# Optimization experiments

Measured on AMD Instinct MI355X. Metric: run time of the kernel, lower is better.

## Reference

```python
import jax, jax.numpy as jnp
import numpy as np

TOP_K = 2  # moe_top_k


def setup_inputs() -> dict:
    key = jax.random.key(0)
    k0, k1, k2, k3 = jax.random.split(key, 4)
    SL, BS, H, F, E = 2048, 4, 1024, 1024, 8
    x = jax.random.normal(k0, (SL, BS, H), dtype=jnp.float32)
    w_router = jax.random.normal(k1, (H, E), dtype=jnp.float32) * 0.02
    w1 = jax.random.normal(k2, (E, H, F), dtype=jnp.float32) * 0.02  # per-expert map weights
    w2 = jax.random.normal(k3, (E, F, H), dtype=jnp.float32) * 0.02  # per-expert reduce weights
    return {"x": x, "w_router": w_router, "w1": w1, "w2": w2}


def reference(x, w_router, w1, w2):
    # dMoA forward: router -> dropless dispatch -> per-expert map GEMM ->
    # per-expert reduce GEMM -> expert-weighted combine. Dropless = no capacity
    # dropping, so a dense all-experts compute + per-token selection is exactly
    # equivalent in math to the sort/gather/grouped-GEMM/scatter pipeline.
    sl, bs, h = x.shape
    E = w1.shape[0]
    xt = x.reshape(-1, h)  # [T, H], T = sl*bs
    T = xt.shape[0]

    # LearnedRouter: softmax over expert logits, then top-k weights/indices
    scores = jax.nn.softmax(xt @ w_router, axis=-1)       # [T, E]
    expert_weights, top_experts = jax.lax.top_k(scores, TOP_K)  # [T, K]

    # load-balancing loss (router.loss): E * sum_e f_e * p_e
    onehot = jax.nn.one_hot(top_experts, E, dtype=xt.dtype)  # [T, K, E]
    tokens_frac = onehot.sum(axis=(0, 1)) / (T * TOP_K)      # f_e
    probs_mean = scores.mean(axis=0)                         # p_e
    loss = E * jnp.sum(tokens_frac * probs_mean)

    # map: per-expert linear H->F, select the top-k experts' outputs per token
    y_all = jnp.einsum('th,ehf->tef', xt, w1)                 # [T, E, F]
    h_tk = jnp.take_along_axis(y_all, top_experts[:, :, None], axis=1)  # [T, K, F]

    # reduce: weighted scatter-combine, then per-expert linear F->H
    hw = jnp.einsum('tke,tk,tkf->tef', onehot, expert_weights, h_tk)  # [T, E, F]
    out = jnp.einsum('tef,efh->th', hw, w2)                   # [T, H]
    return out.reshape(sl, bs, h), loss
```

## Files before the change

### kernel.cpp

```cpp
#include <hip/hip_runtime.h>
#include <hip/hip_bf16.h>
#include <stdint.h>


#define HD 1024
#define FD 1024
#define EN 8

typedef __attribute__((ext_vector_type(8))) short bf16x8;
typedef __attribute__((ext_vector_type(4))) float f32x4;

__device__ __forceinline__ void gload16(const void* g, void* l) {
    __builtin_amdgcn_global_load_lds(
        (const __attribute__((address_space(1))) unsigned int*)g,
        (__attribute__((address_space(3))) unsigned int*)l, 16, 0, 0);
}

__device__ __forceinline__ bf16x8 ds_read128(const short* p) {
    bf16x8 r;
    asm volatile("ds_read_b128 %0, %1"
                 : "=v"(r)
                 : "v"((const __attribute__((address_space(3))) short*)p));
    return r;
}

__device__ __forceinline__ ushort f2bf(float v) {
    __hip_bfloat16 h = __float2bfloat16(v);
    return *(ushort*)&h;
}
__device__ __forceinline__ float bf2f(ushort u) {
    unsigned int w = ((unsigned int)u) << 16;
    float f; __builtin_memcpy(&f, &w, 4); return f;
}

__global__ __launch_bounds__(256) void router_kernel(
    const float* __restrict__ x, const float* __restrict__ wrt,
    ushort* __restrict__ xb,
    int* __restrict__ top_e, float* __restrict__ top_w,
    int* __restrict__ counts, float* __restrict__ probsum)
{
    __shared__ int   cnt_s[EN];
    __shared__ float ps_s[EN];
    int tid = threadIdx.x;
    if (tid < EN) { cnt_s[tid] = 0; ps_s[tid] = 0.f; }
    __syncthreads();

    int wid = tid >> 6, lane = tid & 63;
    int t = blockIdx.x * 4 + wid;
    const float4* xr4 = (const float4*)(x + (size_t)t * HD);
    ushort4* xbo = (ushort4*)(xb + (size_t)t * HD);
    float acc[EN];
#pragma unroll
    for (int e = 0; e < EN; e++) acc[e] = 0.f;
#pragma unroll
    for (int it = 0; it < 4; it++) {
        float4 xv = xr4[it * 64 + lane];
        ushort4 o; o.x = f2bf(xv.x); o.y = f2bf(xv.y); o.z = f2bf(xv.z); o.w = f2bf(xv.w);
        xbo[it * 64 + lane] = o;
        int h0 = it * 256 + lane * 4;
        float xs[4] = {xv.x, xv.y, xv.z, xv.w};
#pragma unroll
        for (int j = 0; j < 4; j++) {
            const float4* wp = (const float4*)(wrt + (size_t)(h0 + j) * EN);
            float4 wa = wp[0], wb = wp[1];
            acc[0] += xs[j] * wa.x; acc[1] += xs[j] * wa.y;
            acc[2] += xs[j] * wa.z; acc[3] += xs[j] * wa.w;
            acc[4] += xs[j] * wb.x; acc[5] += xs[j] * wb.y;
            acc[6] += xs[j] * wb.z; acc[7] += xs[j] * wb.w;
        }
    }
#pragma unroll
    for (int off = 32; off >= 1; off >>= 1) {
#pragma unroll
        for (int e = 0; e < EN; e++) acc[e] += __shfl_xor(acc[e], off, 64);
    }
    if (lane == 0) {
        float m = acc[0];
#pragma unroll
        for (int e = 1; e < EN; e++) m = fmaxf(m, acc[e]);
        float p[EN], s = 0.f;
#pragma unroll
        for (int e = 0; e < EN; e++) { p[e] = expf(acc[e] - m); s += p[e]; }
        float inv = 1.f / s;
#pragma unroll
        for (int e = 0; e < EN; e++) p[e] *= inv;
        int e0 = 0;
#pragma unroll
        for (int e = 1; e < EN; e++) if (p[e] > p[e0]) e0 = e;
        int e1 = (e0 == 0) ? 1 : 0;
#pragma unroll
        for (int e = 0; e < EN; e++) {
            if (e == e0) continue;
            if (p[e] > p[e1]) e1 = e;
        }
        top_e[t * 2] = e0;  top_e[t * 2 + 1] = e1;
        top_w[t * 2] = p[e0]; top_w[t * 2 + 1] = p[e1];
        atomicAdd(&cnt_s[e0], 1); atomicAdd(&cnt_s[e1], 1);
#pragma unroll
        for (int e = 0; e < EN; e++) atomicAdd(&ps_s[e], p[e]);
    }
    __syncthreads();
    if (tid < EN) {
        atomicAdd(&counts[tid], cnt_s[tid]);
        atomicAdd(&probsum[tid], ps_s[tid]);
    }
}

__global__ void prep_kernel(const int* __restrict__ counts,
                            const float* __restrict__ probsum,
                            int* __restrict__ offs, float* __restrict__ loss_out)
{
    int off = 0; float loss = 0.f;
    for (int e = 0; e < EN; e++) {
        offs[e] = off;
        off += counts[e];
        loss += ((float)counts[e] / 16384.f) * (probsum[e] / 8192.f);
    }
    offs[EN] = off;
    *loss_out = 8.f * loss;
}

__global__ __launch_bounds__(256) void dispatch_kernel(
    const int* __restrict__ top_e, const float* __restrict__ top_w,
    const int* __restrict__ offs, int* __restrict__ cursor,
    int* __restrict__ tok_list, float* __restrict__ w_list)
{
    int t = blockIdx.x * 256 + threadIdx.x;
    int lane = threadIdx.x & 63;
#pragma unroll
    for (int k = 0; k < 2; k++) {
        int e = top_e[t * 2 + k];
        int idx = 0;
#pragma unroll
        for (int ex = 0; ex < EN; ex++) {
            unsigned long long m = __ballot(e == ex);
            if (e == ex) {
                int cnt = __popcll(m);
                int leader = __ffsll(m) - 1;
                int pos = 0;
                if (lane == leader) pos = atomicAdd(&cursor[ex * 16], cnt);
                pos = __shfl(pos, leader, 64);
                int rank = __popcll(m & ((1ull << lane) - 1ull));
                idx = offs[ex] + pos + rank;
            }
        }
        tok_list[idx] = t * 2 + k;
        w_list[idx] = top_w[t * 2 + k];
    }
}

__global__ __launch_bounds__(256) void transpose_conv_kernel(
    const float* __restrict__ w1, const float* __restrict__ w2,
    ushort* __restrict__ w1b, ushort* __restrict__ w2b)
{
    __shared__ float tile[32][33];
    int bid = blockIdx.x;
    const float* in; ushort* outp;
    if (bid >= 8192) { in = w2; outp = w2b; bid -= 8192; }
    else             { in = w1; outp = w1b; }
    int e  = bid >> 10;
    int t2 = bid & 1023;
    int tb = t2 >> 5;
    int ta = t2 & 31;
    const float* pin = in + ((size_t)e << 20);
    ushort* pout = outp + ((size_t)e << 20);
    int tx = threadIdx.x & 31, ty = threadIdx.x >> 5;
#pragma unroll
    for (int j = 0; j < 4; j++)
        tile[ty + j * 8][tx] = pin[(size_t)(ta * 32 + ty + j * 8) * 1024 + tb * 32 + tx];
    __syncthreads();
#pragma unroll
    for (int j = 0; j < 4; j++)
        pout[(size_t)(tb * 32 + ty + j * 8) * 1024 + ta * 32 + tx] =
            f2bf(tile[tx][ty + j * 8]);
}


#define RDA(ml_, ks_) ds_read128(&lA[cur][wm * 128 + (ml_) * 16 + lo][(((ks_) * 4 + hi) ^ rx) << 3])
#define RDB(n_, ks_)  ds_read128(&lB[cur][wn * 64  + (n_) * 16 + lo][(((ks_) * 4 + hi) ^ rx) << 3])
#define MFMA_Q(mb_, nb_)                                                      \
    do {                                                                      \
        _Pragma("unroll") for (int ks = 0; ks < 2; ks++)                      \
        _Pragma("unroll") for (int ml = 0; ml < 4; ml++)                      \
        _Pragma("unroll") for (int nl = 0; nl < 2; nl++)                      \
            acc[(mb_) + ml][(nb_) + nl] =                                     \
                __builtin_amdgcn_mfma_f32_16x16x32_bf16(                      \
                    a[ml][ks], b[(nb_) + nl][ks], acc[(mb_) + ml][(nb_) + nl],\
                    0, 0, 0);                                                 \
    } while (0)
#define LGK0_FENCE()                                                          \
    do { asm volatile("s_waitcnt lgkmcnt(0)");                                \
         __builtin_amdgcn_sched_barrier(0); } while (0)
#define BOUNDARY()                                                            \
    do { asm volatile("s_waitcnt vmcnt(0)" ::: "memory");                     \
         __builtin_amdgcn_s_barrier();                                        \
         __builtin_amdgcn_sched_barrier(0); } while (0)

__global__ __launch_bounds__(512, 2) void map_gemm(
    const ushort* __restrict__ xb, const ushort* __restrict__ w1b,
    ushort* __restrict__ hbuf,
    const int* __restrict__ tok_list, const float* __restrict__ w_list,
    const int* __restrict__ offs)
{
    __shared__ __align__(16) short lA[2][256][64];
    __shared__ __align__(16) short lB[2][256][64];
    __shared__ int   tok_s[256];
    __shared__ float wt_s[256];

    int g = blockIdx.x;
    int e = g & 7, q = g >> 3, nb = q & 3, rb = q >> 2;
    int base = offs[e], cnt = offs[e + 1] - base;
    int row0 = rb << 8;
    if (row0 >= cnt) return;
    int rem = cnt - row0;
    int tid = threadIdx.x;
    if (tid < 256) {
        int r = row0 + tid; if (r > cnt - 1) r = cnt - 1;
        tok_s[tid] = tok_list[base + r];
        wt_s[tid]  = w_list[base + r];
    }
    __syncthreads();

    int lane = tid & 63, w = tid >> 6;
    int wm = w >> 2, wn = w & 3;
    int w32 = w * 32;
    int lr = lane >> 3;
    int kseg = ((lane & 7) ^ lr) << 3;

    const ushort* pA[4]; const ushort* pB[4];
    const ushort* wbase = w1b + ((size_t)e << 20);
#pragma unroll
    for (int i = 0; i < 4; i++) {
        int rowT = w32 + i * 8 + lr;
        pA[i] = xb + (size_t)(tok_s[rowT] >> 1) * HD + kseg;
        pB[i] = wbase + (size_t)(nb * 256 + rowT) * HD + kseg;
    }

    f32x4 acc[8][4];
#pragma unroll
    for (int m = 0; m < 8; m++)
#pragma unroll
        for (int n = 0; n < 4; n++) acc[m][n] = (f32x4){0.f, 0.f, 0.f, 0.f};

#pragma unroll
    for (int i = 0; i < 4; i++) {
        gload16(pA[i], &lA[0][w32 + i * 8][0]);
        gload16(pB[i], &lB[0][w32 + i * 8][0]);
        pA[i] += 64; pB[i] += 64;
    }
    BOUNDARY();

    int lo = lane & 15, hi = lane >> 4, rx = lane & 7;
    bf16x8 a[4][2], b[4][2];

    for (int t = 0; t < 16; ++t) {
        int cur = t & 1, nxt = cur ^ 1;
        bool pf = (t < 15);
#pragma unroll
        for (int ks = 0; ks < 2; ks++) {
            a[0][ks] = RDA(0, ks); a[1][ks] = RDA(1, ks);
            a[2][ks] = RDA(2, ks); a[3][ks] = RDA(3, ks);
            b[0][ks] = RDB(0, ks); b[1][ks] = RDB(1, ks);
        }
        if (pf) {
            gload16(pA[0], &lA[nxt][w32 + 0][0]);  pA[0] += 64;
            gload16(pB[0], &lB[nxt][w32 + 0][0]);  pB[0] += 64;
            gload16(pA[1], &lA[nxt][w32 + 8][0]);  pA[1] += 64;
            gload16(pB[1], &lB[nxt][w32 + 8][0]);  pB[1] += 64;
        }
        LGK0_FENCE();
        __builtin_amdgcn_s_setprio(1);
        MFMA_Q(0, 0);
        __builtin_amdgcn_s_setprio(0);
        __builtin_amdgcn_sched_barrier(0);
#pragma unroll
        for (int ks = 0; ks < 2; ks++) {
            b[2][ks] = RDB(2, ks); b[3][ks] = RDB(3, ks);
        }
        if (pf) {
            gload16(pA[2], &lA[nxt][w32 + 16][0]); pA[2] += 64;
            gload16(pB[2], &lB[nxt][w32 + 16][0]); pB[2] += 64;
            gload16(pA[3], &lA[nxt][w32 + 24][0]); pA[3] += 64;
            gload16(pB[3], &lB[nxt][w32 + 24][0]); pB[3] += 64;
        }
        LGK0_FENCE();
        __builtin_amdgcn_s_setprio(1);
        MFMA_Q(0, 2);
        __builtin_amdgcn_s_setprio(0);
        __builtin_amdgcn_sched_barrier(0);
#pragma unroll
        for (int ks = 0; ks < 2; ks++) {
            a[0][ks] = RDA(4, ks); a[1][ks] = RDA(5, ks);
            a[2][ks] = RDA(6, ks); a[3][ks] = RDA(7, ks);
        }
        LGK0_FENCE();
        __builtin_amdgcn_s_setprio(1);
        MFMA_Q(4, 2);
        __builtin_amdgcn_s_setprio(0);
        __builtin_amdgcn_sched_barrier(0);
        __builtin_amdgcn_s_setprio(1);
        MFMA_Q(4, 0);
        __builtin_amdgcn_s_setprio(0);
        __builtin_amdgcn_sched_barrier(0);
        BOUNDARY();
    }

    short* ep = (w < 4 ? (short*)lA : (short*)lB) + (w & 3) * 8192;
#pragma unroll
    for (int m = 0; m < 8; m++)
#pragma unroll
        for (int r = 0; r < 4; r++) {
            int row_l = m * 16 + hi * 4 + r;
            int rswz = (row_l & 7) << 4;
            float wgt = wt_s[wm * 128 + row_l];
#pragma unroll
            for (int n = 0; n < 4; n++) {
                int colb = (n * 16 + lo) * 2;
                ep[(row_l * 128 + (colb ^ rswz)) >> 1] = f2bf(acc[m][n][r] * wgt);
            }
        }
    __syncthreads();
    size_t outbase = (size_t)(base + row0);
    int colg0 = (nb << 8) + wn * 64;
#pragma unroll
    for (int j = 0; j < 16; j++) {
        int row_l = j * 8 + (lane >> 3);
        int r_blk = wm * 128 + row_l;
        int sb = ((lane & 7) * 16) ^ ((row_l & 7) << 4);
        bf16x8 v = *(const bf16x8*)&ep[(row_l * 128 + sb) >> 1];
        if (r_blk < rem)
            *(bf16x8*)&hbuf[(outbase + r_blk) * FD + colg0 + (lane & 7) * 8] = v;
    }
}

__global__ __launch_bounds__(512, 2) void reduce_gemm(
    const ushort* __restrict__ hbuf, const ushort* __restrict__ w2b,
    ushort* __restrict__ obuf,
    const int* __restrict__ tok_list, const int* __restrict__ offs)
{
    __shared__ __align__(16) short lA[2][256][64];
    __shared__ __align__(16) short lB[2][256][64];
    __shared__ int tok_s[256];

    int g = blockIdx.x;
    int e = g & 7, q = g >> 3, nb = q & 3, rb = q >> 2;
    int base = offs[e], cnt = offs[e + 1] - base;
    int row0 = rb << 8;
    if (row0 >= cnt) return;
    int rem = cnt - row0;
    int tid = threadIdx.x;
    if (tid < 256) {
        int r = row0 + tid; if (r > cnt - 1) r = cnt - 1;
        tok_s[tid] = tok_list[base + r];
    }
    __syncthreads();

    int lane = tid & 63, w = tid >> 6;
    int wm = w >> 2, wn = w & 3;
    int w32 = w * 32;
    int lr = lane >> 3;
    int kseg = ((lane & 7) ^ lr) << 3;

    const ushort* pA[4]; const ushort* pB[4];
    const ushort* wbase = w2b + ((size_t)e << 20);
#pragma unroll
    for (int i = 0; i < 4; i++) {
        int rowT = w32 + i * 8 + lr;
        int ar = row0 + rowT; if (ar > cnt - 1) ar = cnt - 1;
        pA[i] = hbuf + (size_t)(base + ar) * FD + kseg;
        pB[i] = wbase + (size_t)(nb * 256 + rowT) * FD + kseg;
    }

    f32x4 acc[8][4];
#pragma unroll
    for (int m = 0; m < 8; m++)
#pragma unroll
        for (int n = 0; n < 4; n++) acc[m][n] = (f32x4){0.f, 0.f, 0.f, 0.f};

#pragma unroll
    for (int i = 0; i < 4; i++) {
        gload16(pA[i], &lA[0][w32 + i * 8][0]);
        gload16(pB[i], &lB[0][w32 + i * 8][0]);
        pA[i] += 64; pB[i] += 64;
    }
    BOUNDARY();

    int lo = lane & 15, hi = lane >> 4, rx = lane & 7;
    bf16x8 a[4][2], b[4][2];

    for (int t = 0; t < 16; ++t) {
        int cur = t & 1, nxt = cur ^ 1;
        bool pf = (t < 15);
#pragma unroll
        for (int ks = 0; ks < 2; ks++) {
            a[0][ks] = RDA(0, ks); a[1][ks] = RDA(1, ks);
            a[2][ks] = RDA(2, ks); a[3][ks] = RDA(3, ks);
            b[0][ks] = RDB(0, ks); b[1][ks] = RDB(1, ks);
        }
        if (pf) {
            gload16(pA[0], &lA[nxt][w32 + 0][0]);  pA[0] += 64;
            gload16(pB[0], &lB[nxt][w32 + 0][0]);  pB[0] += 64;
            gload16(pA[1], &lA[nxt][w32 + 8][0]);  pA[1] += 64;
            gload16(pB[1], &lB[nxt][w32 + 8][0]);  pB[1] += 64;
        }
        LGK0_FENCE();
        __builtin_amdgcn_s_setprio(1);
        MFMA_Q(0, 0);
        __builtin_amdgcn_s_setprio(0);
        __builtin_amdgcn_sched_barrier(0);
#pragma unroll
        for (int ks = 0; ks < 2; ks++) {
            b[2][ks] = RDB(2, ks); b[3][ks] = RDB(3, ks);
        }
        if (pf) {
            gload16(pA[2], &lA[nxt][w32 + 16][0]); pA[2] += 64;
            gload16(pB[2], &lB[nxt][w32 + 16][0]); pB[2] += 64;
            gload16(pA[3], &lA[nxt][w32 + 24][0]); pA[3] += 64;
            gload16(pB[3], &lB[nxt][w32 + 24][0]); pB[3] += 64;
        }
        LGK0_FENCE();
        __builtin_amdgcn_s_setprio(1);
        MFMA_Q(0, 2);
        __builtin_amdgcn_s_setprio(0);
        __builtin_amdgcn_sched_barrier(0);
#pragma unroll
        for (int ks = 0; ks < 2; ks++) {
            a[0][ks] = RDA(4, ks); a[1][ks] = RDA(5, ks);
            a[2][ks] = RDA(6, ks); a[3][ks] = RDA(7, ks);
        }
        LGK0_FENCE();
        __builtin_amdgcn_s_setprio(1);
        MFMA_Q(4, 2);
        __builtin_amdgcn_s_setprio(0);
        __builtin_amdgcn_sched_barrier(0);
        __builtin_amdgcn_s_setprio(1);
        MFMA_Q(4, 0);
        __builtin_amdgcn_s_setprio(0);
        __builtin_amdgcn_sched_barrier(0);
        BOUNDARY();
    }

    short* ep = (w < 4 ? (short*)lA : (short*)lB) + (w & 3) * 8192;
#pragma unroll
    for (int m = 0; m < 8; m++)
#pragma unroll
        for (int r = 0; r < 4; r++) {
            int row_l = m * 16 + hi * 4 + r;
            int rswz = (row_l & 7) << 4;
#pragma unroll
            for (int n = 0; n < 4; n++) {
                int colb = (n * 16 + lo) * 2;
                ep[(row_l * 128 + (colb ^ rswz)) >> 1] = f2bf(acc[m][n][r]);
            }
        }
    __syncthreads();
    int colg0 = (nb << 8) + wn * 64;
#pragma unroll
    for (int j = 0; j < 16; j++) {
        int row_l = j * 8 + (lane >> 3);
        int r_blk = wm * 128 + row_l;
        int sb = ((lane & 7) * 16) ^ ((row_l & 7) << 4);
        bf16x8 v = *(const bf16x8*)&ep[(row_l * 128 + sb) >> 1];
        if (r_blk < rem)
            *(bf16x8*)&obuf[(size_t)tok_s[r_blk] * HD + colg0 + (lane & 7) * 8] = v;
    }
}

__global__ __launch_bounds__(256) void combine_kernel(
    const ushort* __restrict__ obuf, float* __restrict__ out)
{
    int g = blockIdx.x * 256 + threadIdx.x;
    int t = g >> 7, c8 = (g & 127) << 3;
    const ushort* p = obuf + (size_t)t * 2048 + c8;
    bf16x8 a = *(const bf16x8*)p;
    bf16x8 b = *(const bf16x8*)(p + 1024);
    float o[8];
#pragma unroll
    for (int i = 0; i < 8; i++)
        o[i] = bf2f((ushort)a[i]) + bf2f((ushort)b[i]);
    float* q = out + (size_t)t * HD + c8;
    *(float4*)q       = (float4){o[0], o[1], o[2], o[3]};
    *(float4*)(q + 4) = (float4){o[4], o[5], o[6], o[7]};
}

extern "C" void kernel_launch(void* const* d_in, const int* in_sizes, int n_in,
                              void* d_out, int out_size, void* d_ws, size_t ws_size,
                              hipStream_t stream)
{
    const float* x   = (const float*)d_in[0];
    const float* wrt = (const float*)d_in[1];
    const float* w1  = (const float*)d_in[2];
    const float* w2  = (const float*)d_in[3];
    float* out = (float*)d_out;

    uint8_t* ws = (uint8_t*)d_ws;
    ushort* xb   = (ushort*)(ws);
    ushort* w1b  = (ushort*)(ws + (16u << 20));
    ushort* obuf = (ushort*)(ws);
    ushort* w2b  = (ushort*)(ws + (32u << 20));
    ushort* hbuf = (ushort*)(ws + (48u << 20));
    uint8_t* p80 = ws + (80u << 20);
    int*   tok_list = (int*)(p80);
    float* w_list   = (float*)(p80 + (64u << 10));
    int*   top_e    = (int*)(p80 + (128u << 10));
    float* top_w    = (float*)(p80 + (192u << 10));
    uint8_t* ctr    = p80 + (256u << 10);
    int*   counts   = (int*)(ctr);
    float* probsum  = (float*)(ctr + 64);
    int*   offs     = (int*)(ctr + 128);
    int*   cursor   = (int*)(ctr + 256);
    float* loss_out = out + 8388608;

    hipMemsetAsync(ctr, 0, 1024, stream);

    router_kernel<<<2048, 256, 0, stream>>>(x, wrt, xb, top_e, top_w, counts, probsum);
    prep_kernel<<<1, 1, 0, stream>>>(counts, probsum, offs, loss_out);
    dispatch_kernel<<<32, 256, 0, stream>>>(top_e, top_w, offs, cursor, tok_list, w_list);
    transpose_conv_kernel<<<16384, 256, 0, stream>>>(w1, w2, w1b, w2b);
    map_gemm<<<1024, 512, 0, stream>>>(xb, w1b, hbuf, tok_list, w_list, offs);
    reduce_gemm<<<1024, 512, 0, stream>>>(hbuf, w2b, obuf, tok_list, offs);
    combine_kernel<<<4096, 256, 0, stream>>>(obuf, out);
}
```

Before: 205.1 us.

## Stage router weights in LDS, widen weight transpose, fold prep into dispatch

The router kernel now stages the router weights in shared memory once per block and handles 16 tokens per block instead of 4, so each block reads the weights from global memory far less often. The weight transpose and bf16 conversion is rewritten to use 64x128 tiles with float4 loads and 16-byte stores, replacing many small 32x32 blocks. The single-thread prep kernel is removed: each dispatch thread recomputes the expert offsets from the counts, and block 0 also writes the loss and the global offsets. Together these cut memory traffic, block count and one kernel launch, at the cost of 32KB of LDS per router block and redundant offset computation in every dispatch thread.

```diff
diff --git a/kernel.cpp b/kernel.cpp
--- a/kernel.cpp
+++ b/kernel.cpp
@@ -39,65 +39,81 @@
     int* __restrict__ top_e, float* __restrict__ top_w,
     int* __restrict__ counts, float* __restrict__ probsum)
 {
+    __shared__ float lw[EN][HD];
     __shared__ int   cnt_s[EN];
     __shared__ float ps_s[EN];
     int tid = threadIdx.x;
+    {
+        const float4* w4p = (const float4*)(wrt + (size_t)tid * 32);
+#pragma unroll
+        for (int q = 0; q < 4; q++) {
+            float4 a = w4p[q * 2], b = w4p[q * 2 + 1];
+            int h = tid * 4 + q;
+            lw[0][h] = a.x; lw[1][h] = a.y; lw[2][h] = a.z; lw[3][h] = a.w;
+            lw[4][h] = b.x; lw[5][h] = b.y; lw[6][h] = b.z; lw[7][h] = b.w;
+        }
+    }
     if (tid < EN) { cnt_s[tid] = 0; ps_s[tid] = 0.f; }
     __syncthreads();
 
     int wid = tid >> 6, lane = tid & 63;
-    int t = blockIdx.x * 4 + wid;
-    const float4* xr4 = (const float4*)(x + (size_t)t * HD);
-    ushort4* xbo = (ushort4*)(xb + (size_t)t * HD);
-    float acc[EN];
-#pragma unroll
-    for (int e = 0; e < EN; e++) acc[e] = 0.f;
-#pragma unroll
-    for (int it = 0; it < 4; it++) {
-        float4 xv = xr4[it * 64 + lane];
-        ushort4 o; o.x = f2bf(xv.x); o.y = f2bf(xv.y); o.z = f2bf(xv.z); o.w = f2bf(xv.w);
-        xbo[it * 64 + lane] = o;
-        int h0 = it * 256 + lane * 4;
-        float xs[4] = {xv.x, xv.y, xv.z, xv.w};
-#pragma unroll
-        for (int j = 0; j < 4; j++) {
-            const float4* wp = (const float4*)(wrt + (size_t)(h0 + j) * EN);
-            float4 wa = wp[0], wb = wp[1];
-            acc[0] += xs[j] * wa.x; acc[1] += xs[j] * wa.y;
-            acc[2] += xs[j] * wa.z; acc[3] += xs[j] * wa.w;
-            acc[4] += xs[j] * wb.x; acc[5] += xs[j] * wb.y;
-            acc[6] += xs[j] * wb.z; acc[7] += xs[j] * wb.w;
-        }
-    }
-#pragma unroll
-    for (int off = 32; off >= 1; off >>= 1) {
-#pragma unroll
-        for (int e = 0; e < EN; e++) acc[e] += __shfl_xor(acc[e], off, 64);
-    }
-    if (lane == 0) {
-        float m = acc[0];
-#pragma unroll
-        for (int e = 1; e < EN; e++) m = fmaxf(m, acc[e]);
-        float p[EN], s = 0.f;
-#pragma unroll
-        for (int e = 0; e < EN; e++) { p[e] = expf(acc[e] - m); s += p[e]; }
-        float inv = 1.f / s;
-#pragma unroll
-        for (int e = 0; e < EN; e++) p[e] *= inv;
-        int e0 = 0;
-#pragma unroll
-        for (int e = 1; e < EN; e++) if (p[e] > p[e0]) e0 = e;
-        int e1 = (e0 == 0) ? 1 : 0;
-#pragma unroll
-        for (int e = 0; e < EN; e++) {
-            if (e == e0) continue;
-            if (p[e] > p[e1]) e1 = e;
-        }
-        top_e[t * 2] = e0;  top_e[t * 2 + 1] = e1;
-        top_w[t * 2] = p[e0]; top_w[t * 2 + 1] = p[e1];
-        atomicAdd(&cnt_s[e0], 1); atomicAdd(&cnt_s[e1], 1);
-#pragma unroll
-        for (int e = 0; e < EN; e++) atomicAdd(&ps_s[e], p[e]);
+#pragma unroll
+    for (int j = 0; j < 4; j++) {
+        int t = blockIdx.x * 16 + wid * 4 + j;
+        const float4* xr4 = (const float4*)(x + (size_t)t * HD);
+        ushort4* xbo = (ushort4*)(xb + (size_t)t * HD);
+        float4 xv[4];
+#pragma unroll
+        for (int it = 0; it < 4; it++) xv[it] = xr4[it * 64 + lane];
+#pragma unroll
+        for (int it = 0; it < 4; it++) {
+            ushort4 o; o.x = f2bf(xv[it].x); o.y = f2bf(xv[it].y);
+            o.z = f2bf(xv[it].z); o.w = f2bf(xv[it].w);
+            xbo[it * 64 + lane] = o;
+        }
+        float acc[EN];
+#pragma unroll
+        for (int e = 0; e < EN; e++) acc[e] = 0.f;
+#pragma unroll
+        for (int it = 0; it < 4; it++) {
+            int h0 = it * 256 + lane * 4;
+#pragma unroll
+            for (int e = 0; e < EN; e++) {
+                float4 w4 = *(const float4*)&lw[e][h0];
+                acc[e] += xv[it].x * w4.x + xv[it].y * w4.y
+                        + xv[it].z * w4.z + xv[it].w * w4.w;
+            }
+        }
+#pragma unroll
+        for (int off = 32; off >= 1; off >>= 1) {
+#pragma unroll
+            for (int e = 0; e < EN; e++) acc[e] += __shfl_xor(acc[e], off, 64);
+        }
+        if (lane == 0) {
+            float m = acc[0];
+#pragma unroll
+            for (int e = 1; e < EN; e++) m = fmaxf(m, acc[e]);
+            float p[EN], s = 0.f;
+#pragma unroll
+            for (int e = 0; e < EN; e++) { p[e] = expf(acc[e] - m); s += p[e]; }
+            float inv = 1.f / s;
+#pragma unroll
+            for (int e = 0; e < EN; e++) p[e] *= inv;
+            int e0 = 0;
+#pragma unroll
+            for (int e = 1; e < EN; e++) if (p[e] > p[e0]) e0 = e;
+            int e1 = (e0 == 0) ? 1 : 0;
+#pragma unroll
+            for (int e = 0; e < EN; e++) {
+                if (e == e0) continue;
+                if (p[e] > p[e1]) e1 = e;
+            }
+            top_e[t * 2] = e0;  top_e[t * 2 + 1] = e1;
+            top_w[t * 2] = p[e0]; top_w[t * 2 + 1] = p[e1];
+            atomicAdd(&cnt_s[e0], 1); atomicAdd(&cnt_s[e1], 1);
+#pragma unroll
+            for (int e = 0; e < EN; e++) atomicAdd(&ps_s[e], p[e]);
+        }
     }
     __syncthreads();
     if (tid < EN) {
@@ -106,25 +122,70 @@
     }
 }
 
-__global__ void prep_kernel(const int* __restrict__ counts,
-                            const float* __restrict__ probsum,
-                            int* __restrict__ offs, float* __restrict__ loss_out)
-{
-    int off = 0; float loss = 0.f;
-    for (int e = 0; e < EN; e++) {
-        offs[e] = off;
-        off += counts[e];
-        loss += ((float)counts[e] / 16384.f) * (probsum[e] / 8192.f);
-    }
-    offs[EN] = off;
-    *loss_out = 8.f * loss;
+__global__ __launch_bounds__(256) void wconv_kernel(
+    const float* __restrict__ w1, const float* __restrict__ w2,
+    ushort* __restrict__ w1b, ushort* __restrict__ w2b)
+{
+    __shared__ float smem[2][32 * 68];
+    int bid = blockIdx.x;
+    int tid = threadIdx.x;
+    const float* in; ushort* outp;
+    if (bid >= 1024) { in = w2; outp = w2b; bid -= 1024; }
+    else             { in = w1; outp = w1b; }
+    int e   = bid >> 7;
+    int rm  = bid & 127;
+    int kt  = rm >> 3;
+    int ntg = rm & 7;
+    const float* pin = in + ((size_t)e << 20) + (size_t)(kt * 64) * 1024 + ntg * 128;
+    ushort* pout = outp + ((size_t)e << 20) + (size_t)(ntg * 128) * 1024 + kt * 64;
+
+    int kk0 = tid >> 3, c4 = tid & 7;
+    int kk1 = kk0 + 32;
+    int n_r = tid >> 3, ks = (tid & 7) * 8;
+
+    float4 v[8];
+#pragma unroll
+    for (int t = 0; t < 4; t++) {
+        v[2 * t]     = *(const float4*)(pin + (size_t)kk0 * 1024 + t * 32 + c4 * 4);
+        v[2 * t + 1] = *(const float4*)(pin + (size_t)kk1 * 1024 + t * 32 + c4 * 4);
+    }
+#pragma unroll
+    for (int t = 0; t < 4; t++) {
+        float* buf = smem[t & 1];
+        float* d0 = &buf[(c4 * 4) * 68 + kk0];
+        float* d1 = &buf[(c4 * 4) * 68 + kk1];
+        d0[0] = v[2 * t].x; d0[68] = v[2 * t].y; d0[136] = v[2 * t].z; d0[204] = v[2 * t].w;
+        d1[0] = v[2 * t + 1].x; d1[68] = v[2 * t + 1].y; d1[136] = v[2 * t + 1].z; d1[204] = v[2 * t + 1].w;
+        __syncthreads();
+        float4 f0 = *(const float4*)&buf[n_r * 68 + ks];
+        float4 f1 = *(const float4*)&buf[n_r * 68 + ks + 4];
+        ushort us[8];
+        us[0] = f2bf(f0.x); us[1] = f2bf(f0.y); us[2] = f2bf(f0.z); us[3] = f2bf(f0.w);
+        us[4] = f2bf(f1.x); us[5] = f2bf(f1.y); us[6] = f2bf(f1.z); us[7] = f2bf(f1.w);
+        *(uint4*)(pout + (size_t)(t * 32 + n_r) * 1024 + ks) = *(uint4*)us;
+    }
 }
 
 __global__ __launch_bounds__(256) void dispatch_kernel(
+    const int* __restrict__ counts, const float* __restrict__ probsum,
     const int* __restrict__ top_e, const float* __restrict__ top_w,
-    const int* __restrict__ offs, int* __restrict__ cursor,
-    int* __restrict__ tok_list, float* __restrict__ w_list)
-{
+    int* __restrict__ cursor, int* __restrict__ tok_list,
+    float* __restrict__ w_list, int* __restrict__ offs_g,
+    float* __restrict__ loss_out)
+{
+    int offs[EN + 1]; offs[0] = 0;
+#pragma unroll
+    for (int e = 0; e < EN; e++) offs[e + 1] = offs[e] + counts[e];
+    if (blockIdx.x == 0 && threadIdx.x == 0) {
+        float loss = 0.f;
+#pragma unroll
+        for (int e = 0; e < EN; e++) {
+            offs_g[e] = offs[e];
+            loss += ((float)counts[e] / 16384.f) * (probsum[e] / 8192.f);
+        }
+        offs_g[EN] = offs[EN];
+        *loss_out = 8.f * loss;
+    }
     int t = blockIdx.x * 256 + threadIdx.x;
     int lane = threadIdx.x & 63;
 #pragma unroll
@@ -148,33 +209,6 @@
         w_list[idx] = top_w[t * 2 + k];
     }
 }
-
-__global__ __launch_bounds__(256) void transpose_conv_kernel(
-    const float* __restrict__ w1, const float* __restrict__ w2,
-    ushort* __restrict__ w1b, ushort* __restrict__ w2b)
-{
-    __shared__ float tile[32][33];
-    int bid = blockIdx.x;
-    const float* in; ushort* outp;
-    if (bid >= 8192) { in = w2; outp = w2b; bid -= 8192; }
-    else             { in = w1; outp = w1b; }
-    int e  = bid >> 10;
-    int t2 = bid & 1023;
-    int tb = t2 >> 5;
-    int ta = t2 & 31;
-    const float* pin = in + ((size_t)e << 20);
-    ushort* pout = outp + ((size_t)e << 20);
-    int tx = threadIdx.x & 31, ty = threadIdx.x >> 5;
-#pragma unroll
-    for (int j = 0; j < 4; j++)
-        tile[ty + j * 8][tx] = pin[(size_t)(ta * 32 + ty + j * 8) * 1024 + tb * 32 + tx];
-    __syncthreads();
-#pragma unroll
-    for (int j = 0; j < 4; j++)
-        pout[(size_t)(tb * 32 + ty + j * 8) * 1024 + ta * 32 + tx] =
-            f2bf(tile[tx][ty + j * 8]);
-}
-
 
 #define RDA(ml_, ks_) ds_read128(&lA[cur][wm * 128 + (ml_) * 16 + lo][(((ks_) * 4 + hi) ^ rx) << 3])
 #define RDB(n_, ks_)  ds_read128(&lB[cur][wn * 64  + (n_) * 16 + lo][(((ks_) * 4 + hi) ^ rx) << 3])
@@ -513,10 +547,10 @@
 
     hipMemsetAsync(ctr, 0, 1024, stream);
 
-    router_kernel<<<2048, 256, 0, stream>>>(x, wrt, xb, top_e, top_w, counts, probsum);
-    prep_kernel<<<1, 1, 0, stream>>>(counts, probsum, offs, loss_out);
-    dispatch_kernel<<<32, 256, 0, stream>>>(top_e, top_w, offs, cursor, tok_list, w_list);
-    transpose_conv_kernel<<<16384, 256, 0, stream>>>(w1, w2, w1b, w2b);
+    router_kernel<<<512, 256, 0, stream>>>(x, wrt, xb, top_e, top_w, counts, probsum);
+    wconv_kernel<<<2048, 256, 0, stream>>>(w1, w2, w1b, w2b);
+    dispatch_kernel<<<32, 256, 0, stream>>>(counts, probsum, top_e, top_w,
+                                            cursor, tok_list, w_list, offs, loss_out);
     map_gemm<<<1024, 512, 0, stream>>>(xb, w1b, hbuf, tok_list, w_list, offs);
     reduce_gemm<<<1024, 512, 0, stream>>>(hbuf, w2b, obuf, tok_list, offs);
     combine_kernel<<<4096, 256, 0, stream>>>(obuf, out);
```

After: 182.6 us. 10.9% less time.
